# Kernel optimization log

Measured on AMD Instinct MI355X. Metric: run time of the kernel, lower is better.

## Reference

```python
import jax, jax.numpy as jnp
import numpy as np
from jax import lax

STRIDE = (1, 1)
PADDING = ((1, 1), (1, 1))
DILATION = (1, 1)


def setup_inputs() -> dict:
    key = jax.random.key(0)
    k1, k2 = jax.random.split(key)
    input = jax.random.normal(k1, (32, 128, 56, 56), dtype=jnp.float32)
    weight = jax.random.normal(k2, (256, 128, 3, 3), dtype=jnp.float32)
    bias = jnp.zeros((256,), dtype=jnp.float32)
    return {"input": input, "weight": weight, "bias": bias}


def reference(input, weight, bias):
    # The original builds the conv's dense matrix via conv2d on an identity
    # basis and then matmuls; that is mathematically identical to a direct
    # conv2d (the map is linear), plus the broadcast bias.
    out = lax.conv_general_dilated(
        input, weight,
        window_strides=STRIDE,
        padding=PADDING,
        rhs_dilation=DILATION,
        dimension_numbers=("NCHW", "OIHW", "NCHW"),
    )
    return out + bias[None, :, None, None]
```

## Files before the change

### kernel.cpp

```cpp
#include <hip/hip_runtime.h>
#include <hip/hip_bf16.h>
#include <stdint.h>


typedef __attribute__((ext_vector_type(8))) short bf16x8;
typedef __attribute__((ext_vector_type(8))) unsigned short ushort8;
typedef __attribute__((ext_vector_type(4))) float f32x4;

#define HW      56
#define SPATIAL 3136
#define C_IN    128
#define K_OUT   256
#define GEMM_K  1152
#define GEMM_N  100352

#define BM 128
#define BN 256
#define BK 32
#define NT 36
#define BUF_HALVES 12288
#define LB_OFF 4096

__device__ __forceinline__ unsigned short f2bf(float f) {
    union { float f; unsigned int u; } v; v.f = f;
    unsigned int u = v.u + 0x7FFFu + ((v.u >> 16) & 1u);
    return (unsigned short)(u >> 16);
}

__device__ __forceinline__ void gload16(const unsigned short* g, unsigned short* l) {
    __builtin_amdgcn_global_load_lds(
        (const __attribute__((address_space(1))) unsigned int*)(g),
        (__attribute__((address_space(3))) unsigned int*)(l),
        16, 0, 0);
}

__global__ void wtrans_kernel(const float* __restrict__ w, unsigned short* __restrict__ w2) {
    int idx = blockIdx.x * 256 + threadIdx.x;
    int ko  = idx / GEMM_K;
    int r   = idx % GEMM_K;
    int tap = r >> 7;
    int c   = r & 127;
    w2[idx] = f2bf(w[(ko * C_IN + c) * 9 + tap]);
}

__global__ __launch_bounds__(256)
void intrans_kernel(const float* __restrict__ in, unsigned short* __restrict__ nhwc) {
    __shared__ __attribute__((aligned(16))) unsigned short l[56 * 136];
    const int bx = blockIdx.x;
    const int n = bx / HW, h = bx % HW;
    const int tid = threadIdx.x;
    const float* src = in + (size_t)n * C_IN * SPATIAL + h * HW;
    #pragma unroll
    for (int i = 0; i < 28; ++i) {
        int idx = i * 256 + tid;
        int c = idx / HW, w = idx % HW;
        l[w * 136 + c] = f2bf(src[(size_t)c * SPATIAL + w]);
    }
    __syncthreads();
    unsigned short* dst = nhwc + ((size_t)(n * HW + h) * HW) * C_IN;
    #pragma unroll
    for (int j = 0; j < 4; ++j) {
        int chunk = j * 256 + tid;
        if (chunk < 896) {
            int w = chunk >> 4, c8 = chunk & 15;
            *reinterpret_cast<ushort8*>(dst + w * C_IN + c8 * 8) =
                *reinterpret_cast<const ushort8*>(&l[w * 136 + c8 * 8]);
        }
    }
}

__global__ __launch_bounds__(256, 2)
void conv_mfma_pipe(const unsigned short* __restrict__ nhwc,
                    const unsigned short* __restrict__ w2,
                    const unsigned short* __restrict__ zbuf,
                    const float* __restrict__ bias,
                    float* __restrict__ out) {
    __shared__ __attribute__((aligned(16))) unsigned short lds[3 * BUF_HALVES];

    const int tid  = threadIdx.x;
    const int wave = tid >> 6;
    const int lane = tid & 63;
    const int la   = lane & 15;
    const int lkh  = lane >> 4;

    const int bid = blockIdx.y * 392 + blockIdx.x;
    const int swz = (bid & 7) * 98 + (bid >> 3);
    const int m0  = (swz / 392) * BM;
    const int g0  = (swz % 392) * BN;

    const unsigned short* wsrc[2];
    #pragma unroll
    for (int ja = 0; ja < 2; ++ja)
        wsrc[ja] = w2 + (size_t)(m0 + ja * 64 + wave * 16 + (lane >> 2)) * GEMM_K
                      + (lane & 3) * 8;
    int ohs[4], ows[4], pb[4];
    #pragma unroll
    for (int jb = 0; jb < 4; ++jb) {
        int col  = g0 + jb * 64 + wave * 16 + (lane >> 2);
        int nimg = col / SPATIAL;
        int pos  = col - nimg * SPATIAL;
        int oh   = pos / HW;
        int ow   = pos - oh * HW;
        ohs[jb] = oh; ows[jb] = ow;
        pb[jb]  = ((nimg * HW + oh) * HW + ow) * C_IN;
    }
    const int gq = (lane & 3) * 8;

    f32x4 acc[8][4];
    #pragma unroll
    for (int i = 0; i < 8; ++i)
        #pragma unroll
        for (int j = 0; j < 4; ++j)
            acc[i][j] = (f32x4){0.f, 0.f, 0.f, 0.f};

    auto STAGE = [&](int s, int bufi) {
        const int tap = s >> 2, ci = (s & 3) * 32;
        const int dr = tap / 3 - 1, dsx = tap % 3 - 1;
        unsigned short* bA = &lds[bufi * BUF_HALVES];
        unsigned short* bB = bA + LB_OFF;
        #pragma unroll
        for (int ja = 0; ja < 2; ++ja)
            gload16(wsrc[ja] + tap * C_IN + ci, bA + (ja * 64 + wave * 16) * BK);
        const int doff = (dr * HW + dsx) * C_IN + ci;
        #pragma unroll
        for (int jb = 0; jb < 4; ++jb) {
            const int ih = ohs[jb] + dr, iw = ows[jb] + dsx;
            const bool valid = ((unsigned)ih < HW) && ((unsigned)iw < HW);
            const unsigned short* src = valid ? nhwc + pb[jb] + doff + gq
                                              : zbuf + gq;
            gload16(src, bB + (jb * 64 + wave * 16) * BK);
        }
    };

    STAGE(0, 0); STAGE(1, 1); STAGE(2, 2);

    int cur = 0;
    for (int t = 0; t < NT; ++t) {
        if (t <= NT - 3)      asm volatile("s_waitcnt vmcnt(12)" ::: "memory");
        else if (t == NT - 2) asm volatile("s_waitcnt vmcnt(6)"  ::: "memory");
        else                  asm volatile("s_waitcnt vmcnt(0)"  ::: "memory");
        __builtin_amdgcn_s_barrier();
        asm volatile("" ::: "memory");

        const unsigned short* A = &lds[cur * BUF_HALVES];
        const unsigned short* B = A + LB_OFF;
        bf16x8 af[8], bv[4];
        #pragma unroll
        for (int mi = 0; mi < 8; ++mi)
            af[mi] = *reinterpret_cast<const bf16x8*>(&A[(mi * 16 + la) * BK + lkh * 8]);
        #pragma unroll
        for (int nj = 0; nj < 4; ++nj)
            bv[nj] = *reinterpret_cast<const bf16x8*>(&B[(wave * 64 + nj * 16 + la) * BK + lkh * 8]);

        __builtin_amdgcn_s_setprio(1);
        #pragma unroll
        for (int mi = 0; mi < 8; ++mi)
            #pragma unroll
            for (int nj = 0; nj < 4; ++nj)
                acc[mi][nj] = __builtin_amdgcn_mfma_f32_16x16x32_bf16(
                    af[mi], bv[nj], acc[mi][nj], 0, 0, 0);
        __builtin_amdgcn_s_setprio(0);

        asm volatile("s_waitcnt lgkmcnt(0)" ::: "memory");
        __builtin_amdgcn_s_barrier();
        asm volatile("" ::: "memory");

        if (t < NT - 3) STAGE(t + 3, cur);
        cur = (cur == 2) ? 0 : cur + 1;
    }

    #pragma unroll
    for (int mi = 0; mi < 8; ++mi) {
        const f32x4 bv4 = *reinterpret_cast<const f32x4*>(&bias[m0 + mi * 16 + lkh * 4]);
        #pragma unroll
        for (int nj = 0; nj < 4; ++nj) {
            const int gcol = g0 + wave * 64 + nj * 16;
            const int n2 = gcol / SPATIAL;
            const int p2 = gcol - n2 * SPATIAL + la;
            float* op = out + ((size_t)(n2 * K_OUT + m0 + mi * 16 + lkh * 4)) * SPATIAL + p2;
            op[0]               = acc[mi][nj][0] + bv4[0];
            op[SPATIAL]         = acc[mi][nj][1] + bv4[1];
            op[2 * SPATIAL]     = acc[mi][nj][2] + bv4[2];
            op[3 * (size_t)SPATIAL] = acc[mi][nj][3] + bv4[3];
        }
    }
}

#define LDK 40
__global__ __launch_bounds__(256)
void conv_mfma_fallback(const float* __restrict__ in,
                        const float* __restrict__ wraw,
                        const float* __restrict__ bias,
                        float* __restrict__ out) {
    __shared__ __attribute__((aligned(16))) unsigned short lA[BM * LDK];
    __shared__ __attribute__((aligned(16))) unsigned short lB[128 * LDK];
    const int tid = threadIdx.x;
    const int m0  = blockIdx.y * BM;
    const int g0  = blockIdx.x * 128;
    const int wave = tid >> 6, lane = tid & 63;
    const int wr = wave >> 1, wc = wave & 1;
    const int la = lane & 15, lkh = lane >> 4, lk = lkh * 8;

    f32x4 acc[4][4];
    #pragma unroll
    for (int i = 0; i < 4; ++i)
        #pragma unroll
        for (int j = 0; j < 4; ++j)
            acc[i][j] = (f32x4){0.f, 0.f, 0.f, 0.f};

    const int jj = tid & 127;
    const int kb = (tid >> 7) * 16;
    const int g = g0 + jj;
    const int nimg = g / SPATIAL;
    const int pos  = g % SPATIAL;
    const int oh = pos / HW, ow = pos % HW;

    for (int tap = 0; tap < 9; ++tap) {
        const int dr = tap / 3 - 1, dsx = tap % 3 - 1;
        const int ih = oh + dr, iw = ow + dsx;
        const bool valid = ((unsigned)ih < HW) && ((unsigned)iw < HW);
        const float* src = in + ((nimg * C_IN) * HW + ih) * HW + iw;
        for (int c0 = 0; c0 < C_IN; c0 += 32) {
            #pragma unroll
            for (int i = 0; i < 2; ++i) {
                const int ch = tid * 2 + i;
                const int row = ch >> 2;
                const int kp = (ch & 3) * 8;
                ushort8 v;
                #pragma unroll
                for (int e = 0; e < 8; ++e)
                    v[e] = f2bf(wraw[((m0 + row) * C_IN + c0 + kp + e) * 9 + tap]);
                *reinterpret_cast<ushort8*>(&lA[row * LDK + kp]) = v;
            }
            {
                ushort8 v0, v1;
                #pragma unroll
                for (int i = 0; i < 8; ++i)
                    v0[i] = f2bf(valid ? src[(c0 + kb + i) * SPATIAL] : 0.f);
                #pragma unroll
                for (int i = 0; i < 8; ++i)
                    v1[i] = f2bf(valid ? src[(c0 + kb + 8 + i) * SPATIAL] : 0.f);
                *reinterpret_cast<ushort8*>(&lB[jj * LDK + kb])     = v0;
                *reinterpret_cast<ushort8*>(&lB[jj * LDK + kb + 8]) = v1;
            }
            __syncthreads();
            bf16x8 af[4], bv[4];
            #pragma unroll
            for (int f = 0; f < 4; ++f) {
                af[f] = *reinterpret_cast<const bf16x8*>(&lA[(wr * 64 + f * 16 + la) * LDK + lk]);
                bv[f] = *reinterpret_cast<const bf16x8*>(&lB[(wc * 64 + f * 16 + la) * LDK + lk]);
            }
            #pragma unroll
            for (int fi = 0; fi < 4; ++fi)
                #pragma unroll
                for (int fj = 0; fj < 4; ++fj)
                    acc[fi][fj] = __builtin_amdgcn_mfma_f32_16x16x32_bf16(
                        af[fi], bv[fj], acc[fi][fj], 0, 0, 0);
            __syncthreads();
        }
    }
    const int mbase = m0 + wr * 64;
    const int cbase = g0 + wc * 64;
    #pragma unroll
    for (int fi = 0; fi < 4; ++fi) {
        float bvv[4];
        #pragma unroll
        for (int r = 0; r < 4; ++r)
            bvv[r] = bias[mbase + fi * 16 + lkh * 4 + r];
        #pragma unroll
        for (int fj = 0; fj < 4; ++fj) {
            const int gcol = cbase + fj * 16 + la;
            const int n2 = gcol / SPATIAL;
            const int p2 = gcol % SPATIAL;
            float* op = out + (size_t)(n2 * K_OUT) * SPATIAL + p2;
            #pragma unroll
            for (int r = 0; r < 4; ++r)
                op[(size_t)(mbase + fi * 16 + lkh * 4 + r) * SPATIAL] = acc[fi][fj][r] + bvv[r];
        }
    }
}

extern "C" void kernel_launch(void* const* d_in, const int* in_sizes, int n_in,
                              void* d_out, int out_size, void* d_ws, size_t ws_size,
                              hipStream_t stream) {
    const float* in   = (const float*)d_in[0];
    const float* w    = (const float*)d_in[1];
    const float* bias = (const float*)d_in[2];
    float* out = (float*)d_out;

    const size_t need_bytes = (294912ull + 12845056ull + 64ull) * 2ull;

    if (ws_size >= need_bytes) {
        unsigned short* w2   = (unsigned short*)d_ws;
        unsigned short* nhwc = w2 + 294912;
        unsigned short* zbuf = nhwc + 12845056;
        wtrans_kernel<<<(K_OUT * GEMM_K) / 256, 256, 0, stream>>>(w, w2);
        intrans_kernel<<<32 * HW, 256, 0, stream>>>(in, nhwc);
        hipMemsetAsync(zbuf, 0, 128, stream);
        dim3 grid(GEMM_N / BN, K_OUT / BM);
        conv_mfma_pipe<<<grid, 256, 0, stream>>>(nhwc, w2, zbuf, bias, out);
    } else {
        dim3 grid(GEMM_N / 128, K_OUT / BM);
        conv_mfma_fallback<<<grid, 256, 0, stream>>>(in, w, bias, out);
    }
}
```

Baseline: 107.2 us.

## Shrink conv tile to 128x128 with 2x2 wave grid and fragment-native LDS layout

Cuts the block tile from 128x256 to 128x128 and arranges the four waves as a 2x2 grid, each owning 64x64 of output, so accumulator registers halve and occupancy can rise to 3 blocks per CU. Global-to-LDS loads now write each 16-row slab in MFMA fragment order, so the fragment reads become contiguous 16-byte lane accesses and the explicit lgkmcnt wait is dropped. The grid is flattened with a new swizzle that pairs the two M tiles, the main loop is fully unrolled, and the transpose kernel's LDS row pitch is changed from 136 to 140. The cost is that each block reuses fewer B columns per A load, so total global and L2 load traffic increases.

```diff
diff --git a/kernel.cpp b/kernel.cpp
--- a/kernel.cpp
+++ b/kernel.cpp
@@ -15,10 +15,10 @@
 #define GEMM_N  100352
 
 #define BM 128
-#define BN 256
+#define BN 128
 #define BK 32
 #define NT 36
-#define BUF_HALVES 12288
+#define BUF_HALVES 8192
 #define LB_OFF 4096
 
 __device__ __forceinline__ unsigned short f2bf(float f) {
@@ -45,7 +45,7 @@
 
 __global__ __launch_bounds__(256)
 void intrans_kernel(const float* __restrict__ in, unsigned short* __restrict__ nhwc) {
-    __shared__ __attribute__((aligned(16))) unsigned short l[56 * 136];
+    __shared__ __attribute__((aligned(16))) unsigned short l[56 * 140];
     const int bx = blockIdx.x;
     const int n = bx / HW, h = bx % HW;
     const int tid = threadIdx.x;
@@ -54,7 +54,7 @@
     for (int i = 0; i < 28; ++i) {
         int idx = i * 256 + tid;
         int c = idx / HW, w = idx % HW;
-        l[w * 136 + c] = f2bf(src[(size_t)c * SPATIAL + w]);
+        l[w * 140 + c] = f2bf(src[(size_t)c * SPATIAL + w]);
     }
     __syncthreads();
     unsigned short* dst = nhwc + ((size_t)(n * HW + h) * HW) * C_IN;
@@ -64,12 +64,12 @@
         if (chunk < 896) {
             int w = chunk >> 4, c8 = chunk & 15;
             *reinterpret_cast<ushort8*>(dst + w * C_IN + c8 * 8) =
-                *reinterpret_cast<const ushort8*>(&l[w * 136 + c8 * 8]);
-        }
-    }
-}
-
-__global__ __launch_bounds__(256, 2)
+                *reinterpret_cast<const ushort8*>(&l[w * 140 + c8 * 8]);
+        }
+    }
+}
+
+__global__ __launch_bounds__(256, 3)
 void conv_mfma_pipe(const unsigned short* __restrict__ nhwc,
                     const unsigned short* __restrict__ w2,
                     const unsigned short* __restrict__ zbuf,
@@ -82,21 +82,23 @@
     const int lane = tid & 63;
     const int la   = lane & 15;
     const int lkh  = lane >> 4;
-
-    const int bid = blockIdx.y * 392 + blockIdx.x;
-    const int swz = (bid & 7) * 98 + (bid >> 3);
-    const int m0  = (swz / 392) * BM;
-    const int g0  = (swz % 392) * BN;
+    const int gq   = lkh * 8;
+
+    const int bid = blockIdx.x;
+    const int swz = (bid & 7) * 196 + (bid >> 3);
+    const int m0  = (swz & 1) * BM;
+    const int g0  = (swz >> 1) * BN;
+
+    const int wr = wave >> 1, wc = wave & 1;
 
     const unsigned short* wsrc[2];
     #pragma unroll
     for (int ja = 0; ja < 2; ++ja)
-        wsrc[ja] = w2 + (size_t)(m0 + ja * 64 + wave * 16 + (lane >> 2)) * GEMM_K
-                      + (lane & 3) * 8;
-    int ohs[4], ows[4], pb[4];
-    #pragma unroll
-    for (int jb = 0; jb < 4; ++jb) {
-        int col  = g0 + jb * 64 + wave * 16 + (lane >> 2);
+        wsrc[ja] = w2 + (size_t)(m0 + (ja * 4 + wave) * 16 + la) * GEMM_K + gq;
+    int ohs[2], ows[2], pb[2];
+    #pragma unroll
+    for (int jb = 0; jb < 2; ++jb) {
+        int col  = g0 + (jb * 4 + wave) * 16 + la;
         int nimg = col / SPATIAL;
         int pos  = col - nimg * SPATIAL;
         int oh   = pos / HW;
@@ -104,11 +106,10 @@
         ohs[jb] = oh; ows[jb] = ow;
         pb[jb]  = ((nimg * HW + oh) * HW + ow) * C_IN;
     }
-    const int gq = (lane & 3) * 8;
-
-    f32x4 acc[8][4];
-    #pragma unroll
-    for (int i = 0; i < 8; ++i)
+
+    f32x4 acc[4][4];
+    #pragma unroll
+    for (int i = 0; i < 4; ++i)
         #pragma unroll
         for (int j = 0; j < 4; ++j)
             acc[i][j] = (f32x4){0.f, 0.f, 0.f, 0.f};
@@ -118,69 +119,70 @@
         const int dr = tap / 3 - 1, dsx = tap % 3 - 1;
         unsigned short* bA = &lds[bufi * BUF_HALVES];
         unsigned short* bB = bA + LB_OFF;
+        const int wofs = tap * C_IN + ci;
         #pragma unroll
         for (int ja = 0; ja < 2; ++ja)
-            gload16(wsrc[ja] + tap * C_IN + ci, bA + (ja * 64 + wave * 16) * BK);
-        const int doff = (dr * HW + dsx) * C_IN + ci;
-        #pragma unroll
-        for (int jb = 0; jb < 4; ++jb) {
+            gload16(wsrc[ja] + wofs, bA + (ja * 4 + wave) * 512);
+        const int doff = (dr * HW + dsx) * C_IN + ci + gq;
+        #pragma unroll
+        for (int jb = 0; jb < 2; ++jb) {
             const int ih = ohs[jb] + dr, iw = ows[jb] + dsx;
             const bool valid = ((unsigned)ih < HW) && ((unsigned)iw < HW);
-            const unsigned short* src = valid ? nhwc + pb[jb] + doff + gq
-                                              : zbuf + gq;
-            gload16(src, bB + (jb * 64 + wave * 16) * BK);
+            const unsigned short* src = valid ? nhwc + pb[jb] + doff : zbuf + gq;
+            gload16(src, bB + (jb * 4 + wave) * 512);
         }
     };
 
     STAGE(0, 0); STAGE(1, 1); STAGE(2, 2);
 
-    int cur = 0;
+    #pragma unroll
     for (int t = 0; t < NT; ++t) {
-        if (t <= NT - 3)      asm volatile("s_waitcnt vmcnt(12)" ::: "memory");
-        else if (t == NT - 2) asm volatile("s_waitcnt vmcnt(6)"  ::: "memory");
-        else                  asm volatile("s_waitcnt vmcnt(0)"  ::: "memory");
+        if (t < NT - 2)       asm volatile("s_waitcnt vmcnt(8)" ::: "memory");
+        else if (t == NT - 2) asm volatile("s_waitcnt vmcnt(4)" ::: "memory");
+        else                  asm volatile("s_waitcnt vmcnt(0)" ::: "memory");
         __builtin_amdgcn_s_barrier();
         asm volatile("" ::: "memory");
 
+        const int cur = t % 3;
         const unsigned short* A = &lds[cur * BUF_HALVES];
         const unsigned short* B = A + LB_OFF;
-        bf16x8 af[8], bv[4];
-        #pragma unroll
-        for (int mi = 0; mi < 8; ++mi)
-            af[mi] = *reinterpret_cast<const bf16x8*>(&A[(mi * 16 + la) * BK + lkh * 8]);
+        bf16x8 af[4], bv[4];
+        #pragma unroll
+        for (int mi = 0; mi < 4; ++mi)
+            af[mi] = *reinterpret_cast<const bf16x8*>(&A[((wr * 4 + mi) * 64 + lane) * 8]);
         #pragma unroll
         for (int nj = 0; nj < 4; ++nj)
-            bv[nj] = *reinterpret_cast<const bf16x8*>(&B[(wave * 64 + nj * 16 + la) * BK + lkh * 8]);
+            bv[nj] = *reinterpret_cast<const bf16x8*>(&B[((wc * 4 + nj) * 64 + lane) * 8]);
 
         __builtin_amdgcn_s_setprio(1);
         #pragma unroll
-        for (int mi = 0; mi < 8; ++mi)
+        for (int mi = 0; mi < 4; ++mi)
             #pragma unroll
             for (int nj = 0; nj < 4; ++nj)
                 acc[mi][nj] = __builtin_amdgcn_mfma_f32_16x16x32_bf16(
                     af[mi], bv[nj], acc[mi][nj], 0, 0, 0);
         __builtin_amdgcn_s_setprio(0);
 
-        asm volatile("s_waitcnt lgkmcnt(0)" ::: "memory");
         __builtin_amdgcn_s_barrier();
         asm volatile("" ::: "memory");
 
         if (t < NT - 3) STAGE(t + 3, cur);
-        cur = (cur == 2) ? 0 : cur + 1;
-    }
-
-    #pragma unroll
-    for (int mi = 0; mi < 8; ++mi) {
-        const f32x4 bv4 = *reinterpret_cast<const f32x4*>(&bias[m0 + mi * 16 + lkh * 4]);
+    }
+
+    const int mb = m0 + wr * 64;
+    const int cb = g0 + wc * 64;
+    #pragma unroll
+    for (int mi = 0; mi < 4; ++mi) {
+        const f32x4 bv4 = *reinterpret_cast<const f32x4*>(&bias[mb + mi * 16 + lkh * 4]);
         #pragma unroll
         for (int nj = 0; nj < 4; ++nj) {
-            const int gcol = g0 + wave * 64 + nj * 16;
+            const int gcol = cb + nj * 16;
             const int n2 = gcol / SPATIAL;
             const int p2 = gcol - n2 * SPATIAL + la;
-            float* op = out + ((size_t)(n2 * K_OUT + m0 + mi * 16 + lkh * 4)) * SPATIAL + p2;
-            op[0]               = acc[mi][nj][0] + bv4[0];
-            op[SPATIAL]         = acc[mi][nj][1] + bv4[1];
-            op[2 * SPATIAL]     = acc[mi][nj][2] + bv4[2];
+            float* op = out + ((size_t)(n2 * K_OUT + mb + mi * 16 + lkh * 4)) * SPATIAL + p2;
+            op[0]                   = acc[mi][nj][0] + bv4[0];
+            op[SPATIAL]             = acc[mi][nj][1] + bv4[1];
+            op[2 * SPATIAL]         = acc[mi][nj][2] + bv4[2];
             op[3 * (size_t)SPATIAL] = acc[mi][nj][3] + bv4[3];
         }
     }
@@ -297,8 +299,7 @@
         wtrans_kernel<<<(K_OUT * GEMM_K) / 256, 256, 0, stream>>>(w, w2);
         intrans_kernel<<<32 * HW, 256, 0, stream>>>(in, nhwc);
         hipMemsetAsync(zbuf, 0, 128, stream);
-        dim3 grid(GEMM_N / BN, K_OUT / BM);
-        conv_mfma_pipe<<<grid, 256, 0, stream>>>(nhwc, w2, zbuf, bias, out);
+        conv_mfma_pipe<<<(GEMM_N / BN) * (K_OUT / BM), 256, 0, stream>>>(nhwc, w2, zbuf, bias, out);
     } else {
         dim3 grid(GEMM_N / 128, K_OUT / BM);
         conv_mfma_fallback<<<grid, 256, 0, stream>>>(in, w, bias, out);
```

Measured after the change: 144.6 us. 34.9% more time.
